# Optimization experiments

Hardware: AMD Instinct MI355X
Metric: run time of the kernel (lower is better)

The kernel has to match this reference:

```python
import jax, jax.numpy as jnp
import numpy as np

PHI = (1.0 + 5.0 ** 0.5) / 2.0
LUT_N = 4096
TWO_PI = 2.0 * float(np.pi)
B, S, V, D, H = 16, 2048, 4096, 32, 4
DH = D // H


def _lut_tables():
    ang = jnp.arange(LUT_N, dtype=jnp.float32) * (TWO_PI / LUT_N)
    return jnp.sin(ang), jnp.cos(ang)


def _lookup(theta, sin_t, cos_t):
    # LUT sin/cos with linear interpolation (keeps the op differentiable,
    # as a trainable LUT-trig module must be)
    pos = (theta % TWO_PI) * (LUT_N / TWO_PI)
    i0f = jnp.floor(pos)
    f = pos - i0f
    i0 = i0f.astype(jnp.int32) % LUT_N
    i1 = (i0 + 1) % LUT_N
    s = sin_t[i0] * (1.0 - f) + sin_t[i1] * f
    c = cos_t[i0] * (1.0 - f) + cos_t[i1] * f
    return s, c


def setup_inputs() -> dict:
    key = jax.random.key(0)
    ks = jax.random.split(key, 6)
    input_ids = jax.random.randint(ks[0], (B, S), 0, V)
    emb_table = jax.random.normal(ks[1], (V, 2 * D), dtype=jnp.float32) * 0.1
    W_out = jax.random.normal(ks[2], (V, 2 * D), dtype=jnp.float32) * 0.02
    b_out = jnp.zeros((V,), dtype=jnp.float32)
    W_gate = jax.random.normal(ks[3], (2 * D, H), dtype=jnp.float32) * 0.1
    b_gate = jnp.zeros((H,), dtype=jnp.float32)
    decay_logit = jax.random.normal(ks[4], (H,), dtype=jnp.float32)
    echo_scale = jnp.full((1,), 0.5, dtype=jnp.float32)
    return {"input_ids": input_ids, "emb_table": emb_table, "W_out": W_out,
            "b_out": b_out, "W_gate": W_gate, "b_gate": b_gate,
            "decay_logit": decay_logit, "echo_scale": echo_scale}


def _forward(input_ids, emb_table, W_out, b_out, W_gate, b_gate, decay_logit, echo_scale):
    sin_t, cos_t = _lut_tables()
    emb = emb_table[input_ids]                            # [B,S,2D]
    w_seq = jnp.transpose(emb[:, :, :D], (1, 0, 2))       # [S,B,D] frequency half
    b_seq = jnp.transpose(emb[:, :, D:], (1, 0, 2))       # [S,B,D] phase half
    t_phi = jnp.arange(S, dtype=jnp.float32) * PHI        # [S]
    decay = jax.nn.sigmoid(decay_logit)                   # [H] learned memory decay
    es = echo_scale[0]

    def step(carry, inp):
        h_r, h_i, m_r, m_i = carry
        w_t, b_t, tp = inp
        # Euler LUT-trig rotation of the complex state
        wav = 1.0 + jnp.abs(w_t)
        th_r = h_r / wav + b_t + tp
        th_i = h_i / wav + b_t + tp
        s_r, c_r = _lookup(th_r, sin_t, cos_t)
        s_i, c_i = _lookup(th_i, sin_t, cos_t)
        h_r = c_r * c_i - s_r * s_i
        h_i = c_r * s_i + s_r * c_i
        # Echo Chamber: gated per-head write, learned decay, additive read
        gate = jax.nn.sigmoid(jnp.concatenate([h_r, h_i], axis=-1) @ W_gate + b_gate)  # [B,H]
        m_r = decay[None, :, None] * m_r + gate[:, :, None] * h_r.reshape(B, H, DH)
        m_i = decay[None, :, None] * m_i + gate[:, :, None] * h_i.reshape(B, H, DH)
        out_r = h_r + es * m_r.reshape(B, D)
        out_i = h_i + es * m_i.reshape(B, D)
        comb = jnp.concatenate([out_r, out_i], axis=-1)   # [B,2D]
        return (h_r, h_i, m_r, m_i), comb

    init = (jnp.zeros((B, D), jnp.float32), jnp.zeros((B, D), jnp.float32),
            jnp.zeros((B, H, DH), jnp.float32), jnp.zeros((B, H, DH), jnp.float32))
    _, combs = jax.lax.scan(step, init, (w_seq, b_seq, t_phi))  # [S,B,2D]
    logits = jnp.einsum('sbd,vd->sbv', combs, W_out) + b_out    # one fused projection
    return jnp.transpose(logits, (1, 0, 2))                      # [B,S,V]


def reference(input_ids, emb_table, W_out, b_out, W_gate, b_gate, decay_logit, echo_scale):
    return _forward(input_ids, emb_table, W_out, b_out, W_gate, b_gate, decay_logit, echo_scale)
```

## Files before the change

### kernel.cpp

```cpp
#include <hip/hip_runtime.h>

#define S_LEN 2048

typedef float f32x4 __attribute__((ext_vector_type(4)));
typedef int   i32x4 __attribute__((ext_vector_type(4)));
typedef int   i32x2 __attribute__((ext_vector_type(2)));

__device__ __forceinline__ float cos2pi(float rev){ float r; asm("v_cos_f32 %0, %1":"=v"(r):"v"(rev)); return r; }
__device__ __forceinline__ float fractf_(float x){ float r; asm("v_fract_f32 %0, %1":"=v"(r):"v"(x)); return r; }
template<int M>
__device__ __forceinline__ float swz(float x){
  return __int_as_float(__builtin_amdgcn_ds_swizzle(__float_as_int(x), M));
}
template<int CTRL>
__device__ __forceinline__ float dppmov(float x){
  return __int_as_float(__builtin_amdgcn_update_dpp(0, __float_as_int(x), CTRL, 0xf, 0xf, false));
}


__global__ __launch_bounds__(64) void scan_kernel(
    const int* __restrict__ ids, const float* __restrict__ emb,
    const float* __restrict__ Wg, const float* __restrict__ bg,
    const float* __restrict__ dlg, const float* __restrict__ esc,
    ushort* __restrict__ chi, ushort* __restrict__ clo,
    const float* __restrict__ W32, ushort* __restrict__ whi, ushort* __restrict__ wlo)
{
  const int w = blockIdx.x;
  const int l = threadIdx.x;

  if (w >= 512){
    int i0 = (w - 512) * 256 + l * 4;
    int v  = i0 >> 6;
    int q  = (i0 & 63) >> 2;
    int base = v*64 + (q >> 3)*32 + (q & 7);
    float x0 = W32[base], x1 = W32[base+8], x2 = W32[base+16], x3 = W32[base+24];
    unsigned hw01, hw23, lw01, lw23;
    asm("v_cvt_pk_bf16_f32 %0, %1, %2":"=v"(hw01):"v"(x0),"v"(x1));
    asm("v_cvt_pk_bf16_f32 %0, %1, %2":"=v"(hw23):"v"(x2),"v"(x3));
    float r0 = x0 - __uint_as_float(hw01 << 16);
    float r1 = x1 - __uint_as_float(hw01 & 0xffff0000u);
    float r2 = x2 - __uint_as_float(hw23 << 16);
    float r3 = x3 - __uint_as_float(hw23 & 0xffff0000u);
    asm("v_cvt_pk_bf16_f32 %0, %1, %2":"=v"(lw01):"v"(r0),"v"(r1));
    asm("v_cvt_pk_bf16_f32 %0, %1, %2":"=v"(lw23):"v"(r2),"v"(r3));
    *(i32x2*)(whi + i0) = (i32x2){(int)hw01, (int)hw23};
    *(i32x2*)(wlo + i0) = (i32x2){(int)lw01, (int)lw23};
    return;
  }

  const int c  = w >> 4;
  const int b  = w & 15;
  const bool lo = (l < 32);
  const int d  = ((l >> 2) & 7) | ((l & 3) << 3);
  const bool b0 = (l & 1) != 0;
  const bool b1 = (l & 2) != 0;
  const float qoff = lo ? 0.f : 0.25f;

  const float es  = esc[0];
  const int hd = l & 3;
  const float dk  = 1.f/(1.f + __expf(-dlg[hd]));
  const float bgl = bg[hd];
  const int crow = (lo ? 0 : 32) + d;
  const f32x4 wg = *(const f32x4*)(Wg + crow*4);

  const int s0   = c*64;
  const int sw   = (s0 >= 128) ? (s0 - 128) : 0;
  const int send = s0 + 64;
  const int nq   = (send - sw) >> 2;

  const int* idb = ids + b*S_LEN;
  ushort* pch = chi + (size_t)b*S_LEN*64 + l;
  ushort* pcl = clo + (size_t)b*S_LEN*64 + l;

  const float PHI_F   = 1.6180339887498949f;
  const float TWOPI_F = 6.283185307179586f;
  const float INV2PI  = 0.15915494309189535f;

  float h = 0.f, m = 0.f;
  float h1 = 0.f, h2 = 0.f;
  float rev_c, rev_s;
  float q0p, swp;
  float mm1p, psp;
  float w_[4], b_[4], nw_[4], nb_[4];

  auto clampi = [](int x){ return x > (S_LEN-4) ? (S_LEN-4) : x; };

  auto AF = [&](int s, float wv, float bpv){
    float invw = __builtin_amdgcn_rcpf(1.f + __builtin_fabsf(wv));
    float tp = (float)s * PHI_F;
    float th = __builtin_fmaf(h, invw, bpv) + tp;
    float qf = __builtin_floorf(th * INV2PI);
    float r  = __builtin_fmaf(-qf, TWOPI_F, th);
    r = (r < 0.f) ? (r + TWOPI_F) : r;
    r = (r >= TWOPI_F) ? (r - TWOPI_F) : r;
    rev_c = r * INV2PI;
    rev_s = __shfl_xor(rev_c, 32, 64);
  };
  auto AB = [&](){
    float rsum = rev_c + rev_s;
    float hn = cos2pi(fractf_(rsum - qoff));
    h2 = h1; h1 = hn; h = hn;
  };
  auto G0 = [&](){
    float p0 = h1*wg[0], p1 = h1*wg[1], p2 = h1*wg[2], p3 = h1*wg[3];
    float m01 = b0 ? p1 : p0;
    float t01 = b0 ? p0 : p1;
    m01 += dppmov<0xB1>(t01);
    float m23 = b0 ? p3 : p2;
    float t23 = b0 ? p2 : p3;
    m23 += dppmov<0xB1>(t23);
    float mm = b1 ? m23 : m01;
    float tt = b1 ? m01 : m23;
    mm += dppmov<0x4E>(tt);
    mm += dppmov<0x124>(mm);
    mm += dppmov<0x128>(mm);
    q0p = mm;
    swp = swz<0x401F>(mm);
  };
  auto G1 = [&](){
    float mm1 = q0p + swp;
    mm1p = mm1;
    psp = __shfl_xor(mm1, 32, 64);
  };
  auto G2 = [&](int jm2){
    float mm = mm1p + psp;
    float g_ = 1.f / (1.f + __expf(-(mm + bgl)));
    m = __builtin_fmaf(dk, m, g_*h2);
    float outv = __builtin_fmaf(es, m, h2);
    unsigned hw_; asm("v_cvt_pk_bf16_f32 %0, %1, %2" : "=v"(hw_) : "v"(outv), "v"(outv));
    float lr_ = outv - __uint_as_float(hw_ << 16);
    unsigned lw_; asm("v_cvt_pk_bf16_f32 %0, %1, %2" : "=v"(lw_) : "v"(lr_), "v"(lr_));
    if (jm2 >= s0){ pch[jm2*64] = (ushort)hw_; pcl[jm2*64] = (ushort)lw_; }
  };

  {
    i32x4 q0v = *(const i32x4*)(idb + sw);
#pragma unroll
    for (int k=0;k<4;++k){ w_[k] = emb[q0v[k]*64 + d]; b_[k] = emb[q0v[k]*64 + 32 + d]; }
  }
  {
    i32x4 q1v = *(const i32x4*)(idb + clampi(sw + 4));
#pragma unroll
    for (int k=0;k<4;++k){ nw_[k] = emb[q1v[k]*64 + d]; nb_[k] = emb[q1v[k]*64 + 32 + d]; }
  }
  i32x4 qn = *(const i32x4*)(idb + clampi(sw + 8));

  AF(sw,   w_[0], b_[0]); AB();
  AF(sw+1, w_[1], b_[1]); G0(); AB(); G1();

  for (int i = 0; i < nq-1; ++i){
    int j0 = sw + 2 + 4*i;
    AF(j0,   w_[2], b_[2]); G2(j0-2); G0(); AB(); G1();
    AF(j0+1, w_[3], b_[3]); G2(j0-1); G0(); AB(); G1();
#pragma unroll
    for (int k=0;k<4;++k){ w_[k] = nw_[k]; b_[k] = nb_[k]; }
    {
      i32x4 qq = qn;
#pragma unroll
      for (int k=0;k<4;++k){ nw_[k] = emb[qq[k]*64 + d]; nb_[k] = emb[qq[k]*64 + 32 + d]; }
      qn = *(const i32x4*)(idb + clampi(sw + 4*(i+3)));
    }
    AF(j0+2, w_[0], b_[0]); G2(j0);   G0(); AB(); G1();
    AF(j0+3, w_[1], b_[1]); G2(j0+1); G0(); AB(); G1();
  }
  AF(send-2, w_[2], b_[2]); G2(send-4); G0(); AB(); G1();
  AF(send-1, w_[3], b_[3]); G2(send-3); G0(); AB(); G1();
  G2(send-2);
  G0(); G1();
  h2 = h1;
  G2(send-1);
}

__global__ __launch_bounds__(256) void gemm_kernel(
    const ushort* __restrict__ chi, const ushort* __restrict__ clo,
    const ushort* __restrict__ whi, const ushort* __restrict__ wlo,
    const float* __restrict__ bout, float* __restrict__ out)
{
  __shared__ char lds[65536];
  const int row0 = blockIdx.y * 128;
  const int v0   = blockIdx.x * 128;
  const int t = threadIdx.x;

  {
    const char* s0 = (const char*)(chi) + (size_t)row0 * 128;
    const char* s1 = (const char*)(clo) + (size_t)row0 * 128;
    const char* s2 = (const char*)(whi) + (size_t)v0 * 128;
    const char* s3 = (const char*)(wlo) + (size_t)v0 * 128;
    const char* srcs[4] = {s0, s1, s2, s3};
#pragma unroll
    for (int a2 = 0; a2 < 4; ++a2){
      char* dst = lds + a2 * 16384;
      const char* src = srcs[a2];
#pragma unroll
      for (int i = 0; i < 4; ++i){
        int id = t + 256 * i;
        int r = id >> 3, ccol = id & 7;
        i32x4 vv = *(const i32x4*)(src + r*128 + ccol*16);
        *(i32x4*)(dst + r*128 + ((ccol ^ (r & 7)) * 16)) = vv;
      }
    }
  }
  __syncthreads();

  const int lane = t & 63;
  const int wid  = t >> 6;
  const int wr = (wid >> 1) * 64;
  const int wc = (wid & 1) * 64;
  const int lr = lane & 15;
  const int lk = lane >> 4;

  f32x4 acc[4][4];
#pragma unroll
  for (int m = 0; m < 4; ++m)
#pragma unroll
    for (int n = 0; n < 4; ++n) acc[m][n] = (f32x4){0.f, 0.f, 0.f, 0.f};

  i32x2 afr[2][4][4];
#pragma unroll
  for (int hf = 0; hf < 2; ++hf){
    const char* Ab = lds + hf * 16384;
#pragma unroll
    for (int m = 0; m < 4; ++m){
      int row = wr + m*16 + lr;
      const char* rp = Ab + row * 128;
      int sw = (row & 7) << 1;
#pragma unroll
      for (int ks = 0; ks < 4; ++ks){
        int c8 = (ks*4 + lk) ^ sw;
        afr[hf][m][ks] = *(const i32x2*)(rp + c8 * 8);
      }
    }
  }
#pragma unroll
  for (int wh = 0; wh < 2; ++wh){
    const char* Bb = lds + 32768 + wh * 16384;
    i32x2 bfr[4][4];
#pragma unroll
    for (int n = 0; n < 4; ++n){
      int row = wc + n*16 + lr;
      const char* rp = Bb + row * 128;
      int sw = (row & 7) << 1;
#pragma unroll
      for (int ks = 0; ks < 4; ++ks){
        int c8 = (ks*4 + lk) ^ sw;
        bfr[n][ks] = *(const i32x2*)(rp + c8 * 8);
      }
    }
#pragma unroll
    for (int hf = 0; hf < 2; ++hf)
#pragma unroll
      for (int m = 0; m < 4; ++m)
#pragma unroll
        for (int n = 0; n < 4; ++n)
#pragma unroll
          for (int ks = 0; ks < 4; ++ks)
            asm("v_mfma_f32_16x16x16_bf16 %0, %1, %2, %0"
                : "+v"(acc[m][n]) : "v"(afr[hf][m][ks]), "v"(bfr[n][ks]));
  }

#pragma unroll
  for (int n = 0; n < 4; ++n){
    float bias = bout[v0 + wc + n*16 + lr];
#pragma unroll
    for (int m = 0; m < 4; ++m){
      int gr = row0 + wr + m*16 + lk*4;
      float* op = out + (size_t)gr * 4096 + (v0 + wc + n*16 + lr);
#pragma unroll
      for (int rg = 0; rg < 4; ++rg){
        op[(size_t)rg * 4096] = acc[m][n][rg] + bias;
      }
    }
  }
}

extern "C" void kernel_launch(void* const* d_in, const int* in_sizes, int n_in,
                              void* d_out, int out_size, void* d_ws, size_t ws_size,
                              hipStream_t stream)
{
  const int*   ids  = (const int*)  d_in[0];
  const float* emb  = (const float*)d_in[1];
  const float* Wout = (const float*)d_in[2];
  const float* bout = (const float*)d_in[3];
  const float* Wg   = (const float*)d_in[4];
  const float* bg   = (const float*)d_in[5];
  const float* dlg  = (const float*)d_in[6];
  const float* esc  = (const float*)d_in[7];
  float* out = (float*)d_out;
  char* ws = (char*)d_ws;
  ushort* chi = (ushort*)(ws);
  ushort* clo = (ushort*)(ws + 4u*1024u*1024u);
  ushort* whi = (ushort*)(ws + 8u*1024u*1024u);
  ushort* wlo = (ushort*)(ws + 8u*1024u*1024u + 512u*1024u);

  scan_kernel<<<dim3(1536), dim3(64), 0, stream>>>(ids, emb, Wg, bg, dlg, esc,
                                                   chi, clo, Wout, whi, wlo);
  gemm_kernel<<<dim3(32, 256), dim3(256), 0, stream>>>(chi, clo, whi, wlo, bout, out);
}
```

Baseline: 168.8 us.

## Pack two batches per wave with real and imaginary parts in each lane

The scan kernel now gives each lane both the real and imaginary component of one state dimension, so one 64-lane wave handles two batch rows instead of one. This removes the cross-half shuffles (shfl_xor 32) for the rotation and gate reduction, and uses explicit sin and cos evaluation plus complex multiplication in place of the summed-angle cosine trick. Combined outputs are stored as packed 32-bit real/imag pairs, and the W_out bf16 split is permuted to match the new interleaved column layout. It halves the number of scan waves but doubles per-lane ALU work and transcendental calls on the serial dependency chain.

```diff
diff --git a/kernel.cpp b/kernel.cpp
--- a/kernel.cpp
+++ b/kernel.cpp
@@ -6,8 +6,8 @@
 typedef int   i32x4 __attribute__((ext_vector_type(4)));
 typedef int   i32x2 __attribute__((ext_vector_type(2)));
 
+__device__ __forceinline__ float sin2pi(float rev){ float r; asm("v_sin_f32 %0, %1":"=v"(r):"v"(rev)); return r; }
 __device__ __forceinline__ float cos2pi(float rev){ float r; asm("v_cos_f32 %0, %1":"=v"(r):"v"(rev)); return r; }
-__device__ __forceinline__ float fractf_(float x){ float r; asm("v_fract_f32 %0, %1":"=v"(r):"v"(x)); return r; }
 template<int M>
 __device__ __forceinline__ float swz(float x){
   return __int_as_float(__builtin_amdgcn_ds_swizzle(__float_as_int(x), M));
@@ -28,12 +28,15 @@
   const int w = blockIdx.x;
   const int l = threadIdx.x;
 
-  if (w >= 512){
-    int i0 = (w - 512) * 256 + l * 4;
+  if (w >= 256){
+    int i0 = (w - 256) * 256 + l * 4;
     int v  = i0 >> 6;
-    int q  = (i0 & 63) >> 2;
-    int base = v*64 + (q >> 3)*32 + (q & 7);
-    float x0 = W32[base], x1 = W32[base+8], x2 = W32[base+16], x3 = W32[base+24];
+    int ia = (i0 & 63) >> 1;
+    int ib = ia + 1;
+    int da = ((ia >> 2) & 7) | ((ia & 3) << 3);
+    int db = ((ib >> 2) & 7) | ((ib & 3) << 3);
+    float x0 = W32[v*64 + da], x1 = W32[v*64 + 32 + da];
+    float x2 = W32[v*64 + db], x3 = W32[v*64 + 32 + db];
     unsigned hw01, hw23, lw01, lw23;
     asm("v_cvt_pk_bf16_f32 %0, %1, %2":"=v"(hw01):"v"(x0),"v"(x1));
     asm("v_cvt_pk_bf16_f32 %0, %1, %2":"=v"(hw23):"v"(x2),"v"(x3));
@@ -48,20 +51,21 @@
     return;
   }
 
-  const int c  = w >> 4;
-  const int b  = w & 15;
-  const bool lo = (l < 32);
-  const int d  = ((l >> 2) & 7) | ((l & 3) << 3);
+  const int c  = w >> 3;
+  const int bp = w & 7;
+  const int half = l >> 5;
+  const int b  = bp*2 + half;
+  const int i  = l & 31;
+  const int d  = ((i >> 2) & 7) | ((i & 3) << 3);
   const bool b0 = (l & 1) != 0;
   const bool b1 = (l & 2) != 0;
-  const float qoff = lo ? 0.f : 0.25f;
 
   const float es  = esc[0];
   const int hd = l & 3;
   const float dk  = 1.f/(1.f + __expf(-dlg[hd]));
   const float bgl = bg[hd];
-  const int crow = (lo ? 0 : 32) + d;
-  const f32x4 wg = *(const f32x4*)(Wg + crow*4);
+  const f32x4 wgr = *(const f32x4*)(Wg + d*4);
+  const f32x4 wgi = *(const f32x4*)(Wg + (32+d)*4);
 
   const int s0   = c*64;
   const int sw   = (s0 >= 128) ? (s0 - 128) : 0;
@@ -69,40 +73,30 @@
   const int nq   = (send - sw) >> 2;
 
   const int* idb = ids + b*S_LEN;
-  ushort* pch = chi + (size_t)b*S_LEN*64 + l;
-  ushort* pcl = clo + (size_t)b*S_LEN*64 + l;
+  unsigned* pco = (unsigned*)chi + (size_t)b*S_LEN*32 + i;
+  unsigned* plo = (unsigned*)clo + (size_t)b*S_LEN*32 + i;
 
   const float PHI_F   = 1.6180339887498949f;
   const float TWOPI_F = 6.283185307179586f;
   const float INV2PI  = 0.15915494309189535f;
 
-  float h = 0.f, m = 0.f;
-  float h1 = 0.f, h2 = 0.f;
-  float rev_c, rev_s;
-  float q0p, swp;
-  float mm1p, psp;
+  float hr = 0.f, hi = 0.f, mr = 0.f, mi = 0.f;
+  float h2r = 0.f, h2i = 0.f;
+  float mmB = 0.f, swB = 0.f;
   float w_[4], b_[4], nw_[4], nb_[4];
 
   auto clampi = [](int x){ return x > (S_LEN-4) ? (S_LEN-4) : x; };
 
-  auto AF = [&](int s, float wv, float bpv){
-    float invw = __builtin_amdgcn_rcpf(1.f + __builtin_fabsf(wv));
-    float tp = (float)s * PHI_F;
-    float th = __builtin_fmaf(h, invw, bpv) + tp;
-    float qf = __builtin_floorf(th * INV2PI);
-    float r  = __builtin_fmaf(-qf, TWOPI_F, th);
-    r = (r < 0.f) ? (r + TWOPI_F) : r;
-    r = (r >= TWOPI_F) ? (r - TWOPI_F) : r;
-    rev_c = r * INV2PI;
-    rev_s = __shfl_xor(rev_c, 32, 64);
+  auto LOADE = [&](const i32x4& q4, float (&wv)[4], float (&bv)[4]){
+#pragma unroll
+    for (int k=0;k<4;++k){ wv[k] = emb[q4[k]*64 + d]; bv[k] = emb[q4[k]*64 + 32 + d]; }
   };
-  auto AB = [&](){
-    float rsum = rev_c + rev_s;
-    float hn = cos2pi(fractf_(rsum - qoff));
-    h2 = h1; h1 = hn; h = hn;
-  };
-  auto G0 = [&](){
-    float p0 = h1*wg[0], p1 = h1*wg[1], p2 = h1*wg[2], p3 = h1*wg[3];
+
+  auto BODY = [&](int s, float wv, float bpv){
+    float p0 = __builtin_fmaf(hr, wgr[0], hi*wgi[0]);
+    float p1 = __builtin_fmaf(hr, wgr[1], hi*wgi[1]);
+    float p2 = __builtin_fmaf(hr, wgr[2], hi*wgi[2]);
+    float p3 = __builtin_fmaf(hr, wgr[3], hi*wgi[3]);
     float m01 = b0 ? p1 : p0;
     float t01 = b0 ? p0 : p1;
     m01 += dppmov<0xB1>(t01);
@@ -114,61 +108,120 @@
     mm += dppmov<0x4E>(tt);
     mm += dppmov<0x124>(mm);
     mm += dppmov<0x128>(mm);
-    q0p = mm;
-    swp = swz<0x401F>(mm);
+    float invw = __builtin_amdgcn_rcpf(1.f + __builtin_fabsf(wv));
+    float tp = (float)s * PHI_F;
+    float thr = __builtin_fmaf(hr, invw, bpv) + tp;
+    float thi = __builtin_fmaf(hi, invw, bpv) + tp;
+    float qr = __builtin_floorf(thr * INV2PI);
+    float rr = __builtin_fmaf(-qr, TWOPI_F, thr);
+    rr = (rr < 0.f) ? (rr + TWOPI_F) : rr;
+    rr = (rr >= TWOPI_F) ? (rr - TWOPI_F) : rr;
+    float qi = __builtin_floorf(thi * INV2PI);
+    float ri = __builtin_fmaf(-qi, TWOPI_F, thi);
+    ri = (ri < 0.f) ? (ri + TWOPI_F) : ri;
+    ri = (ri >= TWOPI_F) ? (ri - TWOPI_F) : ri;
+    float swA = swz<0x401F>(mm);
+    float sr = sin2pi(rr * INV2PI), cr = cos2pi(rr * INV2PI);
+    float si = sin2pi(ri * INV2PI), ci = cos2pi(ri * INV2PI);
+    float nhr = __builtin_fmaf(cr, ci, -(sr*si));
+    float nhi = __builtin_fmaf(cr, si,  sr*ci);
+    int jm2 = s - 2;
+    if (jm2 >= sw){
+      float z = mmB + swB;
+      float g_ = 1.f / (1.f + __expf(-(z + bgl)));
+      mr = __builtin_fmaf(dk, mr, g_*h2r);
+      mi = __builtin_fmaf(dk, mi, g_*h2i);
+      float outr = __builtin_fmaf(es, mr, h2r);
+      float outi = __builtin_fmaf(es, mi, h2i);
+      unsigned hw_; asm("v_cvt_pk_bf16_f32 %0, %1, %2" : "=v"(hw_) : "v"(outr), "v"(outi));
+      float lr_ = outr - __uint_as_float(hw_ << 16);
+      float li_ = outi - __uint_as_float(hw_ & 0xffff0000u);
+      unsigned lw_; asm("v_cvt_pk_bf16_f32 %0, %1, %2" : "=v"(lw_) : "v"(lr_), "v"(li_));
+      if (jm2 >= s0){ pco[(size_t)jm2*32] = hw_; plo[(size_t)jm2*32] = lw_; }
+    }
+    mmB = mm; swB = swA;
+    h2r = hr; h2i = hi;
+    hr = nhr; hi = nhi;
   };
-  auto G1 = [&](){
-    float mm1 = q0p + swp;
-    mm1p = mm1;
-    psp = __shfl_xor(mm1, 32, 64);
-  };
-  auto G2 = [&](int jm2){
-    float mm = mm1p + psp;
-    float g_ = 1.f / (1.f + __expf(-(mm + bgl)));
-    m = __builtin_fmaf(dk, m, g_*h2);
-    float outv = __builtin_fmaf(es, m, h2);
-    unsigned hw_; asm("v_cvt_pk_bf16_f32 %0, %1, %2" : "=v"(hw_) : "v"(outv), "v"(outv));
-    float lr_ = outv - __uint_as_float(hw_ << 16);
-    unsigned lw_; asm("v_cvt_pk_bf16_f32 %0, %1, %2" : "=v"(lw_) : "v"(lr_), "v"(lr_));
-    if (jm2 >= s0){ pch[jm2*64] = (ushort)hw_; pcl[jm2*64] = (ushort)lw_; }
+
+  auto DRAIN = [&](int sl){
+    float p0 = __builtin_fmaf(hr, wgr[0], hi*wgi[0]);
+    float p1 = __builtin_fmaf(hr, wgr[1], hi*wgi[1]);
+    float p2 = __builtin_fmaf(hr, wgr[2], hi*wgi[2]);
+    float p3 = __builtin_fmaf(hr, wgr[3], hi*wgi[3]);
+    float m01 = b0 ? p1 : p0;
+    float t01 = b0 ? p0 : p1;
+    m01 += dppmov<0xB1>(t01);
+    float m23 = b0 ? p3 : p2;
+    float t23 = b0 ? p2 : p3;
+    m23 += dppmov<0xB1>(t23);
+    float mm = b1 ? m23 : m01;
+    float tt = b1 ? m01 : m23;
+    mm += dppmov<0x4E>(tt);
+    mm += dppmov<0x124>(mm);
+    mm += dppmov<0x128>(mm);
+    float swA = swz<0x401F>(mm);
+    int jm2 = sl - 1;
+    if (jm2 >= sw){
+      float z = mmB + swB;
+      float g_ = 1.f / (1.f + __expf(-(z + bgl)));
+      mr = __builtin_fmaf(dk, mr, g_*h2r);
+      mi = __builtin_fmaf(dk, mi, g_*h2i);
+      float outr = __builtin_fmaf(es, mr, h2r);
+      float outi = __builtin_fmaf(es, mi, h2i);
+      unsigned hw_; asm("v_cvt_pk_bf16_f32 %0, %1, %2" : "=v"(hw_) : "v"(outr), "v"(outi));
+      float lr_ = outr - __uint_as_float(hw_ << 16);
+      float li_ = outi - __uint_as_float(hw_ & 0xffff0000u);
+      unsigned lw_; asm("v_cvt_pk_bf16_f32 %0, %1, %2" : "=v"(lw_) : "v"(lr_), "v"(li_));
+      if (jm2 >= s0){ pco[(size_t)jm2*32] = hw_; plo[(size_t)jm2*32] = lw_; }
+    }
+    mmB = mm; swB = swA;
+    h2r = hr; h2i = hi;
   };
 
   {
     i32x4 q0v = *(const i32x4*)(idb + sw);
-#pragma unroll
-    for (int k=0;k<4;++k){ w_[k] = emb[q0v[k]*64 + d]; b_[k] = emb[q0v[k]*64 + 32 + d]; }
+    LOADE(q0v, w_, b_);
   }
   {
     i32x4 q1v = *(const i32x4*)(idb + clampi(sw + 4));
-#pragma unroll
-    for (int k=0;k<4;++k){ nw_[k] = emb[q1v[k]*64 + d]; nb_[k] = emb[q1v[k]*64 + 32 + d]; }
+    LOADE(q1v, nw_, nb_);
   }
   i32x4 qn = *(const i32x4*)(idb + clampi(sw + 8));
 
-  AF(sw,   w_[0], b_[0]); AB();
-  AF(sw+1, w_[1], b_[1]); G0(); AB(); G1();
-
-  for (int i = 0; i < nq-1; ++i){
-    int j0 = sw + 2 + 4*i;
-    AF(j0,   w_[2], b_[2]); G2(j0-2); G0(); AB(); G1();
-    AF(j0+1, w_[3], b_[3]); G2(j0-1); G0(); AB(); G1();
+  BODY(sw,   w_[0], b_[0]);
+  BODY(sw+1, w_[1], b_[1]);
+
+  for (int it = 0; it < nq-1; ++it){
+    int j0 = sw + 2 + 4*it;
+    BODY(j0,   w_[2], b_[2]);
+    BODY(j0+1, w_[3], b_[3]);
 #pragma unroll
     for (int k=0;k<4;++k){ w_[k] = nw_[k]; b_[k] = nb_[k]; }
     {
       i32x4 qq = qn;
-#pragma unroll
-      for (int k=0;k<4;++k){ nw_[k] = emb[qq[k]*64 + d]; nb_[k] = emb[qq[k]*64 + 32 + d]; }
-      qn = *(const i32x4*)(idb + clampi(sw + 4*(i+3)));
-    }
-    AF(j0+2, w_[0], b_[0]); G2(j0);   G0(); AB(); G1();
-    AF(j0+3, w_[1], b_[1]); G2(j0+1); G0(); AB(); G1();
-  }
-  AF(send-2, w_[2], b_[2]); G2(send-4); G0(); AB(); G1();
-  AF(send-1, w_[3], b_[3]); G2(send-3); G0(); AB(); G1();
-  G2(send-2);
-  G0(); G1();
-  h2 = h1;
-  G2(send-1);
+      LOADE(qq, nw_, nb_);
+      qn = *(const i32x4*)(idb + clampi(sw + 4*(it+3)));
+    }
+    BODY(j0+2, w_[0], b_[0]);
+    BODY(j0+3, w_[1], b_[1]);
+  }
+  BODY(send-2, w_[2], b_[2]);
+  BODY(send-1, w_[3], b_[3]);
+  DRAIN(send-1);
+  {
+    float z = mmB + swB;
+    float g_ = 1.f / (1.f + __expf(-(z + bgl)));
+    mr = __builtin_fmaf(dk, mr, g_*h2r);
+    mi = __builtin_fmaf(dk, mi, g_*h2i);
+    float outr = __builtin_fmaf(es, mr, h2r);
+    float outi = __builtin_fmaf(es, mi, h2i);
+    unsigned hw_; asm("v_cvt_pk_bf16_f32 %0, %1, %2" : "=v"(hw_) : "v"(outr), "v"(outi));
+    float lr_ = outr - __uint_as_float(hw_ << 16);
+    float li_ = outi - __uint_as_float(hw_ & 0xffff0000u);
+    unsigned lw_; asm("v_cvt_pk_bf16_f32 %0, %1, %2" : "=v"(lw_) : "v"(lr_), "v"(li_));
+    pco[(size_t)(send-1)*32] = hw_; plo[(size_t)(send-1)*32] = lw_;
+  }
 }
 
 __global__ __launch_bounds__(256) void gemm_kernel(
@@ -292,7 +345,7 @@
   ushort* whi = (ushort*)(ws + 8u*1024u*1024u);
   ushort* wlo = (ushort*)(ws + 8u*1024u*1024u + 512u*1024u);
 
-  scan_kernel<<<dim3(1536), dim3(64), 0, stream>>>(ids, emb, Wg, bg, dlg, esc,
+  scan_kernel<<<dim3(1280), dim3(64), 0, stream>>>(ids, emb, Wg, bg, dlg, esc,
                                                    chi, clo, Wout, whi, wlo);
   gemm_kernel<<<dim3(32, 256), dim3(256), 0, stream>>>(chi, clo, whi, wlo, bout, out);
 }
```

After: 175.7 us. 1.04x slower.
